# Kernel optimization log

Measured on AMD Instinct MI355X. Metric: run time of the kernel, lower is better.

## Reference

```python
import jax, jax.numpy as jnp
import numpy as np

D_MODEL = 1024
N_HEADS = 16
D_K = D_MODEL // N_HEADS
BATCH = 2
SEQ = 2048


def setup_inputs() -> dict:
    key = jax.random.key(0)
    ks = jax.random.split(key, 9)
    s = 1.0 / np.sqrt(D_MODEL)
    x = jax.random.normal(ks[0], (BATCH, SEQ, D_MODEL), dtype=jnp.float32)
    # nn.Linear params: weight [out, in], bias [out]
    w_q = jax.random.uniform(ks[1], (D_MODEL, D_MODEL), jnp.float32, -s, s)
    b_q = jax.random.uniform(ks[2], (D_MODEL,), jnp.float32, -s, s)
    w_k = jax.random.uniform(ks[3], (D_MODEL, D_MODEL), jnp.float32, -s, s)
    b_k = jax.random.uniform(ks[4], (D_MODEL,), jnp.float32, -s, s)
    w_v = jax.random.uniform(ks[5], (D_MODEL, D_MODEL), jnp.float32, -s, s)
    b_v = jax.random.uniform(ks[6], (D_MODEL,), jnp.float32, -s, s)
    w_o = jax.random.uniform(ks[7], (D_MODEL, D_MODEL), jnp.float32, -s, s)
    b_o = jax.random.uniform(ks[8], (D_MODEL,), jnp.float32, -s, s)
    return {"x": x, "w_q": w_q, "b_q": b_q, "w_k": w_k, "b_k": b_k,
            "w_v": w_v, "b_v": b_v, "w_o": w_o, "b_o": b_o}


def reference(x, w_q, b_q, w_k, b_k, w_v, b_v, w_o, b_o):
    B, S, _ = x.shape
    # Linear projections, then split heads: [B, H, S, d_k]
    def proj(w, b):
        y = jnp.einsum('bsd,ed->bse', x, w) + b
        return y.reshape(B, S, N_HEADS, D_K).transpose(0, 2, 1, 3)
    q = proj(w_q, b_q)
    k = proj(w_k, b_k)
    v = proj(w_v, b_v)
    scores = jnp.einsum('bhqd,bhkd->bhqk', q, k) / jnp.sqrt(jnp.float32(D_K))
    attn = jax.nn.softmax(scores, axis=-1)  # dropout is identity in eval mode
    out = jnp.einsum('bhqk,bhkd->bhqd', attn, v)
    out = out.transpose(0, 2, 1, 3).reshape(B, S, D_MODEL)
    out = jnp.einsum('bsd,ed->bse', out, w_o) + b_o
    return out, attn
```

## Files before the change

### kernel.cpp

```cpp
#include <hip/hip_runtime.h>
#include <hip/hip_bf16.h>
#include <stdint.h>


typedef __attribute__((ext_vector_type(4))) float f32x4;
typedef __attribute__((ext_vector_type(8))) short s16x8;
typedef __attribute__((ext_vector_type(8))) unsigned short u16x8;
typedef __attribute__((ext_vector_type(4))) unsigned short u16x4;

#define MFMA(a, b, c) __builtin_amdgcn_mfma_f32_16x16x32_bf16((a), (b), (c), 0, 0, 0)

__device__ __forceinline__ unsigned short f2bf(float f) {
    unsigned int u = __float_as_uint(f);
    unsigned int r = (u + 0x7FFFu + ((u >> 16) & 1u)) >> 16;
    return (unsigned short)r;
}

__global__ void convert_kernel(const float* __restrict__ x,
                               const float* __restrict__ wq, const float* __restrict__ wk,
                               const float* __restrict__ wv, const float* __restrict__ wo,
                               unsigned short* __restrict__ xb, unsigned short* __restrict__ wb) {
    size_t g = (size_t)blockIdx.x * blockDim.x + threadIdx.x;
    size_t i4 = g * 4;
    const float* src;
    unsigned short* dst;
    size_t off;
    if (i4 < 4194304) {
        src = x; dst = xb; off = i4;
    } else {
        size_t j = i4 - 4194304;
        int wsel = (int)(j >> 20);
        off = j & 1048575;
        src = (wsel == 0) ? wq : (wsel == 1) ? wk : (wsel == 2) ? wv : wo;
        dst = wb + ((size_t)wsel << 20);
    }
    float4 v = *(const float4*)(src + off);
    u16x4 o;
    o[0] = f2bf(v.x); o[1] = f2bf(v.y); o[2] = f2bf(v.z); o[3] = f2bf(v.w);
    *(u16x4*)(dst + off) = o;
}

__global__ __launch_bounds__(256, 3) void gemm_kernel(
    const unsigned short* __restrict__ A, const unsigned short* __restrict__ B,
    const float* __restrict__ bias_q, const float* __restrict__ bias_k,
    const float* __restrict__ bias_v, int mode,
    unsigned short* __restrict__ Qs, unsigned short* __restrict__ Kb,
    unsigned short* __restrict__ Vt, float* __restrict__ outp) {
    const int t = threadIdx.x;
    const int lane = t & 63;
    const int wv4 = t >> 6;
    const int wr = wv4 >> 1, wc = wv4 & 1;
    const int rowbase = blockIdx.y * 128;
    const int colbase = blockIdx.x * 128;

    __shared__ __align__(16) unsigned short lA[128 * 64];
    __shared__ __align__(16) unsigned short lB[128 * 64];

    const int crow = lane >> 3;
    const int ccol = (lane & 7) * 8;

    f32x4 acc[4][4];
#pragma unroll
    for (int mi = 0; mi < 4; ++mi)
#pragma unroll
        for (int ni = 0; ni < 4; ++ni)
            acc[mi][ni] = (f32x4){0.f, 0.f, 0.f, 0.f};

    const int l15 = lane & 15;
    const int koff = (lane >> 4) * 8;
    const int ar = wr * 64 + l15;
    const int br = wc * 64 + l15;

    for (int kt = 0; kt < 16; ++kt) {
        const int kbase = kt * 64 + ccol;
#pragma unroll
        for (int i = 0; i < 4; ++i) {
            const int c = wv4 * 4 + i;
            const int r = c * 8 + crow;
            __builtin_amdgcn_global_load_lds(
                (const __attribute__((address_space(1))) void*)(A + (size_t)(rowbase + r) * 1024 + kbase),
                (__attribute__((address_space(3))) void*)&lA[c * 512], 16, 0, 0);
            __builtin_amdgcn_global_load_lds(
                (const __attribute__((address_space(1))) void*)(B + (size_t)(colbase + r) * 1024 + kbase),
                (__attribute__((address_space(3))) void*)&lB[c * 512], 16, 0, 0);
        }
        __syncthreads();
#pragma unroll
        for (int kk = 0; kk < 2; ++kk) {
            s16x8 af[4], bf[4];
#pragma unroll
            for (int mi = 0; mi < 4; ++mi)
                af[mi] = *(const s16x8*)&lA[(ar + mi * 16) * 64 + kk * 32 + koff];
#pragma unroll
            for (int ni = 0; ni < 4; ++ni)
                bf[ni] = *(const s16x8*)&lB[(br + ni * 16) * 64 + kk * 32 + koff];
#pragma unroll
            for (int mi = 0; mi < 4; ++mi)
#pragma unroll
                for (int ni = 0; ni < 4; ++ni)
                    acc[mi][ni] = MFMA(af[mi], bf[ni], acc[mi][ni]);
        }
        __syncthreads();
    }

    if (mode == 1) {
#pragma unroll
        for (int ni = 0; ni < 4; ++ni) {
            int n = colbase + wc * 64 + ni * 16 + l15;
            float bv = bias_q[n];
#pragma unroll
            for (int mi = 0; mi < 4; ++mi) {
#pragma unroll
                for (int reg = 0; reg < 4; ++reg) {
                    int m = rowbase + wr * 64 + mi * 16 + (lane >> 4) * 4 + reg;
                    outp[(size_t)m * 1024 + n] = acc[mi][ni][reg] + bv;
                }
            }
        }
    } else {
        const int proj = colbase >> 10;
        const float* bias = (proj == 0) ? bias_q : (proj == 1) ? bias_k : bias_v;
        const float scale = (proj == 0) ? 0.18033688011112042f : 1.0f;
#pragma unroll
        for (int ni = 0; ni < 4; ++ni) {
            int n = colbase + wc * 64 + ni * 16 + l15;
            int nn = n & 1023;
            int h = nn >> 6, d = nn & 63;
            float bv = bias[nn];
#pragma unroll
            for (int mi = 0; mi < 4; ++mi) {
                int m0 = rowbase + wr * 64 + mi * 16 + (lane >> 4) * 4;
                int b = m0 >> 11, s0 = m0 & 2047;
                if (proj == 2) {
                    u16x4 pk;
#pragma unroll
                    for (int reg = 0; reg < 4; ++reg)
                        pk[reg] = f2bf(acc[mi][ni][reg] + bv);
                    int j0 = s0 & 31;
                    int pg = (j0 >> 2) & 3, pn = (j0 >> 4) & 1;
                    int pcol = (s0 & ~31) | (pg << 3) | (pn << 2);
                    *(u16x4*)&Vt[((size_t)(b * 16 + h) * 64 + d) * 2048 + pcol] = pk;
                } else {
                    unsigned short* dstp = (proj == 0) ? Qs : Kb;
#pragma unroll
                    for (int reg = 0; reg < 4; ++reg)
                        dstp[((size_t)(b * 16 + h) * 2048 + (s0 + reg)) * 64 + d] =
                            f2bf((acc[mi][ni][reg] + bv) * scale);
                }
            }
        }
    }
}

__global__ __launch_bounds__(256, 2) void attn_kernel(
    const unsigned short* __restrict__ Qs, const unsigned short* __restrict__ Kb,
    const unsigned short* __restrict__ Vt, float* __restrict__ attn,
    unsigned short* __restrict__ ctx) {
    const int t = threadIdx.x;
    const int lane = t & 63;
    const int l15 = lane & 15;
    const int g = lane >> 4;
    const int g4 = g * 4, g8 = g * 8;
    const int w = t >> 6;
    const int wr = w >> 1, wc = w & 1;
    const int qt = blockIdx.x;
    const int bh = blockIdx.y;
    const int b = bh >> 4, h = bh & 15;

    const unsigned short* Qh = Qs + (size_t)bh * (2048 * 64);
    const unsigned short* Kh = Kb + (size_t)bh * (2048 * 64);
    const unsigned short* Vh = Vt + (size_t)bh * (64 * 2048);
    float* attn_h = attn + (size_t)bh * (2048 * 2048) + (size_t)(qt * 128) * 2048;

    __shared__ float lred[2][128];
    __shared__ float lO[2][64 * 65];

    s16x8 qf[8];
#pragma unroll
    for (int mi = 0; mi < 4; ++mi)
#pragma unroll
        for (int kk = 0; kk < 2; ++kk)
            qf[mi * 2 + kk] =
                *(const s16x8*)&Qh[(size_t)(qt * 128 + wr * 64 + mi * 16 + l15) * 64 + kk * 32 + g8];

    s16x8 kf0[4], kf1[4], vf0[4], vf1[4];

#define K_LOAD(DST, KT)                                                                     \
    {                                                                                       \
        _Pragma("unroll") for (int ni = 0; ni < 2; ++ni)                                    \
            _Pragma("unroll") for (int kk = 0; kk < 2; ++kk)                                \
                DST[ni * 2 + kk] = *(const s16x8*)&Kh[(size_t)((KT) * 64 + wc * 32 +        \
                                                               ni * 16 + l15) * 64 +        \
                                                      kk * 32 + g8];                        \
    }
#define V_LOAD(DST, KT)                                                                     \
    {                                                                                       \
        _Pragma("unroll") for (int db = 0; db < 4; ++db)                                    \
            DST[db] = *(const s16x8*)&Vh[(size_t)(db * 16 + l15) * 2048 +                   \
                                         (KT) * 64 + wc * 32 + g8];                         \
    }
#define QK_MFMA(KF, SACC)                                                                   \
    {                                                                                       \
        _Pragma("unroll") for (int kk = 0; kk < 2; ++kk)                                    \
            _Pragma("unroll") for (int mi = 0; mi < 4; ++mi)                                \
                _Pragma("unroll") for (int ni = 0; ni < 2; ++ni)                            \
                    SACC[mi][ni] = MFMA(KF[ni * 2 + kk], qf[mi * 2 + kk], SACC[mi][ni]);    \
    }

    float qsum[4] = {0.f, 0.f, 0.f, 0.f};
    K_LOAD(kf0, 0);
#define P1_BODY(KF, KFN, KT)                                                                \
    {                                                                                       \
        f32x4 sacc[4][2];                                                                   \
        _Pragma("unroll") for (int mi = 0; mi < 4; ++mi)                                    \
            _Pragma("unroll") for (int ni = 0; ni < 2; ++ni)                                \
                sacc[mi][ni] = (f32x4){0.f, 0.f, 0.f, 0.f};                                 \
        QK_MFMA(KF, sacc);                                                                  \
        if ((KT) < 31) K_LOAD(KFN, (KT) + 1);                                               \
        _Pragma("unroll") for (int mi = 0; mi < 4; ++mi) {                                  \
            float e = 0.f;                                                                  \
            _Pragma("unroll") for (int ni = 0; ni < 2; ++ni)                                \
                _Pragma("unroll") for (int r = 0; r < 4; ++r)                               \
                    e += exp2f(sacc[mi][ni][r]);                                            \
            qsum[mi] += e;                                                                  \
        }                                                                                   \
    }
    for (int k2 = 0; k2 < 16; ++k2) {
        P1_BODY(kf0, kf1, 2 * k2);
        P1_BODY(kf1, kf0, 2 * k2 + 1);
    }
#pragma unroll
    for (int mi = 0; mi < 4; ++mi) {
        float v = qsum[mi];
        v += __shfl_xor(v, 16);
        v += __shfl_xor(v, 32);
        qsum[mi] = v;
    }
    if (lane < 16) {
#pragma unroll
        for (int mi = 0; mi < 4; ++mi)
            lred[wc][wr * 64 + mi * 16 + lane] = qsum[mi];
    }
    __syncthreads();
    float rl[4];
#pragma unroll
    for (int mi = 0; mi < 4; ++mi) {
        int q = wr * 64 + mi * 16 + l15;
        rl[mi] = 1.0f / (lred[0][q] + lred[1][q]);
    }

    f32x4 oacc[4][4];
#pragma unroll
    for (int mi = 0; mi < 4; ++mi)
#pragma unroll
        for (int db = 0; db < 4; ++db) oacc[mi][db] = (f32x4){0.f, 0.f, 0.f, 0.f};

    K_LOAD(kf0, 0);
    V_LOAD(vf0, 0);
#define P2_BODY(KF, KFN, VF, VFN, KT)                                                       \
    {                                                                                       \
        f32x4 sacc[4][2];                                                                   \
        _Pragma("unroll") for (int mi = 0; mi < 4; ++mi)                                    \
            _Pragma("unroll") for (int ni = 0; ni < 2; ++ni)                                \
                sacc[mi][ni] = (f32x4){0.f, 0.f, 0.f, 0.f};                                 \
        QK_MFMA(KF, sacc);                                                                  \
        if ((KT) < 31) {                                                                    \
            K_LOAD(KFN, (KT) + 1);                                                          \
            V_LOAD(VFN, (KT) + 1);                                                          \
        }                                                                                   \
        s16x8 pf[4];                                                                        \
        _Pragma("unroll") for (int mi = 0; mi < 4; ++mi) {                                  \
            const int q = wr * 64 + mi * 16 + l15;                                          \
            u16x8 pk;                                                                       \
            _Pragma("unroll") for (int ni = 0; ni < 2; ++ni) {                              \
                float4 pv;                                                                  \
                pv.x = exp2f(sacc[mi][ni][0]) * rl[mi];                                     \
                pv.y = exp2f(sacc[mi][ni][1]) * rl[mi];                                     \
                pv.z = exp2f(sacc[mi][ni][2]) * rl[mi];                                     \
                pv.w = exp2f(sacc[mi][ni][3]) * rl[mi];                                     \
                *(float4*)&attn_h[(size_t)q * 2048 + (KT) * 64 + wc * 32 + ni * 16 + g4] =  \
                    pv;                                                                     \
                pk[ni * 4 + 0] = f2bf(pv.x);                                                \
                pk[ni * 4 + 1] = f2bf(pv.y);                                                \
                pk[ni * 4 + 2] = f2bf(pv.z);                                                \
                pk[ni * 4 + 3] = f2bf(pv.w);                                                \
            }                                                                               \
            pf[mi] = *(const s16x8*)&pk;                                                    \
        }                                                                                   \
        _Pragma("unroll") for (int mi = 0; mi < 4; ++mi)                                    \
            _Pragma("unroll") for (int db = 0; db < 4; ++db)                                \
                oacc[mi][db] = MFMA(pf[mi], VF[db], oacc[mi][db]);                          \
    }
    for (int k2 = 0; k2 < 16; ++k2) {
        P2_BODY(kf0, kf1, vf0, vf1, 2 * k2);
        P2_BODY(kf1, kf0, vf1, vf0, 2 * k2 + 1);
    }

    if (wc == 1) {
#pragma unroll
        for (int mi = 0; mi < 4; ++mi)
#pragma unroll
            for (int db = 0; db < 4; ++db)
#pragma unroll
                for (int r = 0; r < 4; ++r)
                    lO[wr][(mi * 16 + g4 + r) * 65 + db * 16 + l15] = oacc[mi][db][r];
    }
    __syncthreads();
    if (wc == 0) {
#pragma unroll
        for (int mi = 0; mi < 4; ++mi) {
#pragma unroll
            for (int db = 0; db < 4; ++db) {
#pragma unroll
                for (int r = 0; r < 4; ++r) {
                    float s = oacc[mi][db][r] + lO[wr][(mi * 16 + g4 + r) * 65 + db * 16 + l15];
                    int q = qt * 128 + wr * 64 + mi * 16 + g4 + r;
                    ctx[((size_t)(b * 2048 + q)) * 1024 + h * 64 + db * 16 + l15] = f2bf(s);
                }
            }
        }
    }
#undef K_LOAD
#undef V_LOAD
#undef QK_MFMA
#undef P1_BODY
#undef P2_BODY
}

extern "C" void kernel_launch(void* const* d_in, const int* in_sizes, int n_in,
                              void* d_out, int out_size, void* d_ws, size_t ws_size,
                              hipStream_t stream) {
    const float* x  = (const float*)d_in[0];
    const float* wq = (const float*)d_in[1];
    const float* bq = (const float*)d_in[2];
    const float* wk = (const float*)d_in[3];
    const float* bk = (const float*)d_in[4];
    const float* wv = (const float*)d_in[5];
    const float* bv = (const float*)d_in[6];
    const float* wo = (const float*)d_in[7];
    const float* bo = (const float*)d_in[8];

    char* ws = (char*)d_ws;
    unsigned short* xb  = (unsigned short*)(ws);
    unsigned short* wb  = (unsigned short*)(ws + 8388608);
    unsigned short* Qsc = (unsigned short*)(ws + 16777216);
    unsigned short* Kb  = (unsigned short*)(ws + 25165824);
    unsigned short* Vt  = (unsigned short*)(ws + 33554432);
    unsigned short* ctx = (unsigned short*)(ws + 41943040);

    float* out  = (float*)d_out;
    float* attn = out + 4194304;

    convert_kernel<<<8192, 256, 0, stream>>>(x, wq, wk, wv, wo, xb, wb);
    gemm_kernel<<<dim3(24, 32), 256, 0, stream>>>(xb, wb, bq, bk, bv, 0,
                                                  Qsc, Kb, Vt, nullptr);
    attn_kernel<<<dim3(16, 32), 256, 0, stream>>>(Qsc, Kb, Vt, attn, ctx);
    gemm_kernel<<<dim3(8, 32), 256, 0, stream>>>(ctx, wb + 3 * 1048576, bo, bo, bo, 1,
                                                 nullptr, nullptr, nullptr, out);
}
```

Baseline: 283.3 us.

## Stage attention probabilities in LDS for coalesced row-wise global stores

```diff
diff --git a/kernel.cpp b/kernel.cpp
--- a/kernel.cpp
+++ b/kernel.cpp
@@ -14,6 +14,9 @@
     unsigned int u = __float_as_uint(f);
     unsigned int r = (u + 0x7FFFu + ((u >> 16) & 1u)) >> 16;
     return (unsigned short)r;
+}
+__device__ __forceinline__ float bf2f(unsigned short v) {
+    return __uint_as_float(((unsigned int)v) << 16);
 }
 
 __global__ void convert_kernel(const float* __restrict__ x,
@@ -172,8 +175,9 @@
     const unsigned short* Vh = Vt + (size_t)bh * (64 * 2048);
     float* attn_h = attn + (size_t)bh * (2048 * 2048) + (size_t)(qt * 128) * 2048;
 
+    __shared__ unsigned short P_lds[128 * 264];
     __shared__ float lred[2][128];
-    __shared__ float lO[2][64 * 65];
+    float* lOp = (float*)P_lds;
 
     s16x8 qf[8];
 #pragma unroll
@@ -273,27 +277,45 @@
             const int q = wr * 64 + mi * 16 + l15;                                          \
             u16x8 pk;                                                                       \
             _Pragma("unroll") for (int ni = 0; ni < 2; ++ni) {                              \
-                float4 pv;                                                                  \
-                pv.x = exp2f(sacc[mi][ni][0]) * rl[mi];                                     \
-                pv.y = exp2f(sacc[mi][ni][1]) * rl[mi];                                     \
-                pv.z = exp2f(sacc[mi][ni][2]) * rl[mi];                                     \
-                pv.w = exp2f(sacc[mi][ni][3]) * rl[mi];                                     \
-                *(float4*)&attn_h[(size_t)q * 2048 + (KT) * 64 + wc * 32 + ni * 16 + g4] =  \
-                    pv;                                                                     \
-                pk[ni * 4 + 0] = f2bf(pv.x);                                                \
-                pk[ni * 4 + 1] = f2bf(pv.y);                                                \
-                pk[ni * 4 + 2] = f2bf(pv.z);                                                \
-                pk[ni * 4 + 3] = f2bf(pv.w);                                                \
+                pk[ni * 4 + 0] = f2bf(exp2f(sacc[mi][ni][0]) * rl[mi]);                     \
+                pk[ni * 4 + 1] = f2bf(exp2f(sacc[mi][ni][1]) * rl[mi]);                     \
+                pk[ni * 4 + 2] = f2bf(exp2f(sacc[mi][ni][2]) * rl[mi]);                     \
+                pk[ni * 4 + 3] = f2bf(exp2f(sacc[mi][ni][3]) * rl[mi]);                     \
             }                                                                               \
+            u16x4 plo, phi;                                                                 \
+            plo[0] = pk[0]; plo[1] = pk[1]; plo[2] = pk[2]; plo[3] = pk[3];                 \
+            phi[0] = pk[4]; phi[1] = pk[5]; phi[2] = pk[6]; phi[3] = pk[7];                 \
+            const int cb = q * 264 + (((KT) & 3) << 6) + wc * 32 + g4;                      \
+            *(u16x4*)&P_lds[cb] = plo;                                                      \
+            *(u16x4*)&P_lds[cb + 16] = phi;                                                 \
             pf[mi] = *(const s16x8*)&pk;                                                    \
         }                                                                                   \
         _Pragma("unroll") for (int mi = 0; mi < 4; ++mi)                                    \
             _Pragma("unroll") for (int db = 0; db < 4; ++db)                                \
                 oacc[mi][db] = MFMA(pf[mi], VF[db], oacc[mi][db]);                          \
     }
-    for (int k2 = 0; k2 < 16; ++k2) {
-        P2_BODY(kf0, kf1, vf0, vf1, 2 * k2);
-        P2_BODY(kf1, kf0, vf1, vf0, 2 * k2 + 1);
+#define RAW_BARRIER()                                                                       \
+    asm volatile("s_waitcnt lgkmcnt(0)" ::: "memory");                                      \
+    __builtin_amdgcn_s_barrier();                                                           \
+    __builtin_amdgcn_sched_barrier(0);
+
+    for (int si = 0; si < 8; ++si) {
+        P2_BODY(kf0, kf1, vf0, vf1, si * 4 + 0);
+        P2_BODY(kf1, kf0, vf1, vf0, si * 4 + 1);
+        P2_BODY(kf0, kf1, vf0, vf1, si * 4 + 2);
+        P2_BODY(kf1, kf0, vf1, vf0, si * 4 + 3);
+        RAW_BARRIER();
+        const int sbase = si * 256;
+        const int lx4 = lane * 4;
+#pragma unroll
+        for (int i = 0; i < 32; ++i) {
+            const int r = w * 32 + i;
+            u16x4 pb = *(const u16x4*)&P_lds[r * 264 + lx4];
+            float4 o4;
+            o4.x = bf2f(pb[0]); o4.y = bf2f(pb[1]); o4.z = bf2f(pb[2]); o4.w = bf2f(pb[3]);
+            *(float4*)&attn_h[(size_t)r * 2048 + sbase + lx4] = o4;
+        }
+        RAW_BARRIER();
     }
 
     if (wc == 1) {
@@ -303,7 +325,8 @@
             for (int db = 0; db < 4; ++db)
 #pragma unroll
                 for (int r = 0; r < 4; ++r)
-                    lO[wr][(mi * 16 + g4 + r) * 65 + db * 16 + l15] = oacc[mi][db][r];
+                    lOp[(size_t)wr * 4160 + (mi * 16 + g4 + r) * 65 + db * 16 + l15] =
+                        oacc[mi][db][r];
     }
     __syncthreads();
     if (wc == 0) {
@@ -313,7 +336,8 @@
             for (int db = 0; db < 4; ++db) {
 #pragma unroll
                 for (int r = 0; r < 4; ++r) {
-                    float s = oacc[mi][db][r] + lO[wr][(mi * 16 + g4 + r) * 65 + db * 16 + l15];
+                    float s = oacc[mi][db][r] +
+                              lOp[(size_t)wr * 4160 + (mi * 16 + g4 + r) * 65 + db * 16 + l15];
                     int q = qt * 128 + wr * 64 + mi * 16 + g4 + r;
                     ctx[((size_t)(b * 2048 + q)) * 1024 + h * 64 + db * 16 + l15] = f2bf(s);
                 }
@@ -325,6 +349,7 @@
 #undef QK_MFMA
 #undef P1_BODY
 #undef P2_BODY
+#undef RAW_BARRIER
 }
 
 extern "C" void kernel_launch(void* const* d_in, const int* in_sizes, int n_in,
```

Result: slower. 300.7 us (+6.2%).
